# Kernel optimization log

Measured on AMD Instinct MI355X. Metric: run time of the kernel, lower is better.

Reference implementation:

```python
import jax, jax.numpy as jnp
import numpy as np

B, S, D, H = 8, 1024, 768, 12
DH = D // H  # 64


def setup_inputs() -> dict:
    key = jax.random.key(0)
    ks = jax.random.split(key, 7)
    scale = 0.05
    return {
        "sequences": jax.random.normal(ks[0], (B, S, D), dtype=jnp.float32),
        "Wq": jax.random.normal(ks[1], (H, DH, DH), dtype=jnp.float32) * scale,
        "bq": jax.random.normal(ks[2], (H, DH), dtype=jnp.float32) * scale,
        "Wk": jax.random.normal(ks[3], (H, DH, DH), dtype=jnp.float32) * scale,
        "bk": jax.random.normal(ks[4], (H, DH), dtype=jnp.float32) * scale,
        "Wv": jax.random.normal(ks[5], (H, DH, DH), dtype=jnp.float32) * scale,
        "bv": jax.random.normal(ks[6], (H, DH), dtype=jnp.float32) * scale,
    }


def reference(sequences, Wq, bq, Wk, bk, Wv, bv):
    # sequences: [B, S, D]; per-head slice of width DH gets its own Linear.
    b, s, d = sequences.shape
    h, dh = Wq.shape[0], Wq.shape[-1]
    xh = sequences.reshape(b, s, h, dh)  # [B,S,H,DH] head-chunked features
    q = jnp.einsum('bshd,hde->bshe', xh, Wq) + bq  # [B,S,H,DH]
    k = jnp.einsum('bshd,hde->bshe', xh, Wk) + bk
    v = jnp.einsum('bshd,hde->bshe', xh, Wv) + bv
    scores = jnp.einsum('bqhd,bkhd->bhqk', q, k) / jnp.sqrt(jnp.float32(dh))
    weights = jax.nn.softmax(scores, axis=-1)  # [B,H,S,S]
    out = jnp.einsum('bhqk,bkhd->bqhd', weights, v)  # [B,S,H,DH]
    return out.reshape(b, s, d)  # hstack of heads == reshape back to D
```

## Files before the change

### kernel.cpp

```cpp
#include <hip/hip_runtime.h>
#include <hip/hip_bf16.h>
#include <math.h>

constexpr int Bn = 8, Sn = 1024, Dn = 768, Hn = 12, DHn = 64;
constexpr int QKV_ELEMS = Bn * Hn * Sn * DHn;
constexpr float SQC = 0.42466086f;

typedef __attribute__((ext_vector_type(8))) short bf16x8;
typedef __attribute__((ext_vector_type(4))) float f32x4;

__device__ __forceinline__ unsigned short f2bf(float f) {
    union { float f; unsigned u; } c{f};
    return (unsigned short)((c.u + 0x8000) >> 16);
}
__device__ __forceinline__ unsigned int pk2bf(float a, float b) {
    union { float f; unsigned u; } ca{a}, cb{b};
    return __builtin_amdgcn_perm(cb.u + 0x8000u, ca.u + 0x8000u, 0x07060302u);
}

__global__ __launch_bounds__(256) void prep_kernel(
    const float* __restrict__ Wq, const float* __restrict__ Wk,
    const float* __restrict__ Wv, unsigned short* __restrict__ wt_g)
{
    __shared__ float Ws[64][65];
    const int mh = blockIdx.x;
    const int m  = mh / Hn;
    const int h  = mh % Hn;
    const float* W = (m == 0 ? Wq : (m == 1 ? Wk : Wv)) + (size_t)h * 4096;
    const int t  = threadIdx.x;
    const int r  = t >> 2;
    const int c0 = (t & 3) * 16;
    #pragma unroll
    for (int q4 = 0; q4 < 4; q4++) {
        float4 v = ((const float4*)(W + r * 64 + c0))[q4];
        Ws[r][c0 + 4 * q4 + 0] = v.x;
        Ws[r][c0 + 4 * q4 + 1] = v.y;
        Ws[r][c0 + 4 * q4 + 2] = v.z;
        Ws[r][c0 + 4 * q4 + 3] = v.w;
    }
    __syncthreads();
    const int e  = t >> 2;
    const int d0 = (t & 3) * 16;
    const float sc = (m < 2) ? SQC : 1.0f;
    unsigned short tmp[16];
    #pragma unroll
    for (int j = 0; j < 16; j++) tmp[j] = f2bf(Ws[d0 + j][e] * sc);
    uint4* dst = (uint4*)(wt_g + ((size_t)(mh * 64 + e)) * 64 + d0);
    dst[0] = ((uint4*)tmp)[0];
    dst[1] = ((uint4*)tmp)[1];
}

__global__ __launch_bounds__(256) void proj_kernel(
    const float* __restrict__ x, const unsigned short* __restrict__ wt_g,
    const float* __restrict__ bk, const float* __restrict__ bv,
    unsigned short* __restrict__ k_ws, unsigned short* __restrict__ vt_ws)
{
    __shared__ unsigned short Xs[64 * 72];
    __shared__ unsigned short ObK[64 * 72];
    __shared__ unsigned short ObV[64 * 72];

    const int blk  = blockIdx.x;
    const int tile = blk & 15;
    const int bh   = blk >> 4;
    const int h    = bh % Hn;
    const int b    = bh / Hn;
    const int t    = threadIdx.x;
    const int w    = t >> 6;
    const int lane = t & 63;
    const int l    = lane & 15;
    const int quad = lane >> 4;
    const int r    = t >> 2;
    const int c0   = (t & 3) * 16;
    const int s0   = tile * 64;

    {
        const float* xrow = x + ((size_t)(b * Sn + s0 + r) * Dn + h * 64 + c0);
        unsigned int tmp[8];
        #pragma unroll
        for (int q4 = 0; q4 < 4; q4++) {
            float4 v = ((const float4*)xrow)[q4];
            tmp[2 * q4 + 0] = pk2bf(v.x, v.y);
            tmp[2 * q4 + 1] = pk2bf(v.z, v.w);
        }
        *(uint4*)&Xs[r * 72 + c0]     = ((uint4*)tmp)[0];
        *(uint4*)&Xs[r * 72 + c0 + 8] = ((uint4*)tmp)[1];
    }

    bf16x8 wk[2], wv[2];
    {
        const unsigned short* kp = wt_g + ((size_t)((1 * Hn + h) * 64 + w * 16 + l)) * 64 + quad * 8;
        const unsigned short* vp = wt_g + ((size_t)((2 * Hn + h) * 64 + w * 16 + l)) * 64 + quad * 8;
        uint4 a0 = *(const uint4*)kp;      uint4 a1 = *(const uint4*)(kp + 32);
        uint4 b0 = *(const uint4*)vp;      uint4 b1 = *(const uint4*)(vp + 32);
        wk[0] = *(bf16x8*)&a0; wk[1] = *(bf16x8*)&a1;
        wv[0] = *(bf16x8*)&b0; wv[1] = *(bf16x8*)&b1;
    }
    float4 bkv = *(const float4*)(bk + h * 64 + w * 16 + quad * 4);
    float4 bvv = *(const float4*)(bv + h * 64 + w * 16 + quad * 4);

    __syncthreads();

    bf16x8 xb[4][2];
    #pragma unroll
    for (int nt = 0; nt < 4; nt++)
        #pragma unroll
        for (int kc = 0; kc < 2; kc++)
            xb[nt][kc] = *(bf16x8*)&Xs[(nt * 16 + l) * 72 + kc * 32 + quad * 8];

    f32x4 ak[4], av[4];
    #pragma unroll
    for (int nt = 0; nt < 4; nt++) {
        ak[nt] = (f32x4){bkv.x * SQC, bkv.y * SQC, bkv.z * SQC, bkv.w * SQC};
        av[nt] = (f32x4){bvv.x, bvv.y, bvv.z, bvv.w};
    }
    #pragma unroll
    for (int nt = 0; nt < 4; nt++)
        #pragma unroll
        for (int kc = 0; kc < 2; kc++) {
            ak[nt] = __builtin_amdgcn_mfma_f32_16x16x32_bf16(wk[kc], xb[nt][kc], ak[nt], 0, 0, 0);
            av[nt] = __builtin_amdgcn_mfma_f32_16x16x32_bf16(wv[kc], xb[nt][kc], av[nt], 0, 0, 0);
        }

    #pragma unroll
    for (int nt = 0; nt < 4; nt++) {
        *(uint2*)&ObK[(nt * 16 + l) * 72 + w * 16 + quad * 4] =
            make_uint2(pk2bf(ak[nt][0], ak[nt][1]), pk2bf(ak[nt][2], ak[nt][3]));
        #pragma unroll
        for (int rr = 0; rr < 4; rr++)
            ObV[(w * 16 + quad * 4 + rr) * 72 + nt * 16 + l] = f2bf(av[nt][rr]);
    }
    __syncthreads();

    {
        uint4 a = *(uint4*)&ObK[r * 72 + c0];
        uint4 bq4 = *(uint4*)&ObK[r * 72 + c0 + 8];
        unsigned short* dst = k_ws + (size_t)(bh * Sn + s0 + r) * 64 + c0;
        ((uint4*)dst)[0] = a;
        *(uint4*)(dst + 8) = bq4;
    }
    {
        uint4 a = *(uint4*)&ObV[r * 72 + c0];
        uint4 bq4 = *(uint4*)&ObV[r * 72 + c0 + 8];
        unsigned short* dst = vt_ws + (size_t)bh * 64 * Sn + (size_t)r * Sn + s0 + c0;
        ((uint4*)dst)[0] = a;
        *(uint4*)(dst + 8) = bq4;
    }
}

__global__ __launch_bounds__(256) void attn_kernel(
    const float* __restrict__ x, const unsigned short* __restrict__ wt_g,
    const float* __restrict__ bq,
    const unsigned short* __restrict__ k_ws,
    const unsigned short* __restrict__ vt_ws,
    float* __restrict__ out)
{
    __shared__ unsigned short Ks[64 * 72];
    __shared__ unsigned short Vt[64 * 72];
    __shared__ unsigned short Pws[4 * 32 * 72];

    const int blk = blockIdx.x;
    const int xcd = blk & 7;
    const int idx = blk >> 3;
    const int bh  = xcd * 12 + (idx % 12);
    const int qt  = idx / 12;
    const int t    = threadIdx.x;
    const int w    = t >> 6;
    const int lane = t & 63;
    const int l    = lane & 15;
    const int quad = lane >> 4;
    const int sr   = t >> 2;
    const int sc0  = (t & 3) * 16;

    const int b = bh / Hn, h = bh % Hn;
    const size_t base  = (size_t)bh * Sn * 64;
    const size_t vbase = (size_t)bh * 64 * Sn;

    unsigned short* Pw = Pws + w * 32 * 72;

    bf16x8 qf[2][2];
    {
        bf16x8 xq[2][2];
        #pragma unroll
        for (int st = 0; st < 2; st++) {
            const float* xp = x + ((size_t)(b * Sn + qt * 128 + w * 32 + st * 16 + l) * Dn
                                   + h * 64 + quad * 8);
            #pragma unroll
            for (int kc = 0; kc < 2; kc++) {
                float4 v0 = *(const float4*)(xp + kc * 32);
                float4 v1 = *(const float4*)(xp + kc * 32 + 4);
                unsigned int tmp[4] = {pk2bf(v0.x, v0.y), pk2bf(v0.z, v0.w),
                                       pk2bf(v1.x, v1.y), pk2bf(v1.z, v1.w)};
                xq[st][kc] = *(bf16x8*)tmp;
            }
        }
        #pragma unroll
        for (int nt = 0; nt < 4; nt++) {
            const unsigned short* wp = wt_g + ((size_t)((0 * Hn + h) * 64 + nt * 16 + l)) * 64 + quad * 8;
            uint4 a0 = *(const uint4*)wp;
            uint4 a1 = *(const uint4*)(wp + 32);
            bf16x8 wa0 = *(bf16x8*)&a0, wa1 = *(bf16x8*)&a1;
            float4 bqv = *(const float4*)(bq + h * 64 + nt * 16 + quad * 4);
            #pragma unroll
            for (int st = 0; st < 2; st++) {
                f32x4 acc = (f32x4){bqv.x * SQC, bqv.y * SQC, bqv.z * SQC, bqv.w * SQC};
                acc = __builtin_amdgcn_mfma_f32_16x16x32_bf16(wa0, xq[st][0], acc, 0, 0, 0);
                acc = __builtin_amdgcn_mfma_f32_16x16x32_bf16(wa1, xq[st][1], acc, 0, 0, 0);
                *(uint2*)&Pw[(st * 16 + l) * 72 + nt * 16 + quad * 4] =
                    make_uint2(pk2bf(acc[0], acc[1]), pk2bf(acc[2], acc[3]));
            }
        }
        __asm__ volatile("s_waitcnt lgkmcnt(0)" ::: "memory");
        #pragma unroll
        for (int st = 0; st < 2; st++) {
            qf[st][0] = *(bf16x8*)&Pw[(st * 16 + l) * 72 + quad * 8];
            qf[st][1] = *(bf16x8*)&Pw[(st * 16 + l) * 72 + 32 + quad * 8];
        }
    }

    f32x4 Oa[2][4];
    #pragma unroll
    for (int st = 0; st < 2; st++)
        #pragma unroll
        for (int nt = 0; nt < 4; nt++) Oa[st][nt] = (f32x4){0.f, 0.f, 0.f, 0.f};
    float ps[2] = {0.f, 0.f};

    for (int kt = 0; kt < 16; kt++) {
        __syncthreads();
        {
            const unsigned short* kp = k_ws + base + (size_t)(kt * 64 + sr) * 64 + sc0;
            uint4 ka = *(const uint4*)kp;
            uint4 kb = *(const uint4*)(kp + 8);
            const unsigned short* vp = vt_ws + vbase + (size_t)sr * Sn + kt * 64 + sc0;
            uint4 va = *(const uint4*)vp;
            uint4 vb = *(const uint4*)(vp + 8);
            *(uint4*)&Ks[sr * 72 + sc0]     = ka;
            *(uint4*)&Ks[sr * 72 + sc0 + 8] = kb;
            *(uint4*)&Vt[sr * 72 + sc0]     = va;
            *(uint4*)&Vt[sr * 72 + sc0 + 8] = vb;
        }
        __syncthreads();

        #pragma unroll
        for (int nt = 0; nt < 4; nt++) {
            bf16x8 kf0 = *(bf16x8*)&Ks[(nt * 16 + l) * 72 + quad * 8];
            bf16x8 kf1 = *(bf16x8*)&Ks[(nt * 16 + l) * 72 + 32 + quad * 8];
            #pragma unroll
            for (int st = 0; st < 2; st++) {
                f32x4 s = (f32x4){0.f, 0.f, 0.f, 0.f};
                s = __builtin_amdgcn_mfma_f32_16x16x32_bf16(kf0, qf[st][0], s, 0, 0, 0);
                s = __builtin_amdgcn_mfma_f32_16x16x32_bf16(kf1, qf[st][1], s, 0, 0, 0);
                float p0 = exp2f(s[0]), p1 = exp2f(s[1]);
                float p2 = exp2f(s[2]), p3 = exp2f(s[3]);
                ps[st] += (p0 + p1) + (p2 + p3);
                *(uint2*)&Pw[(st * 16 + l) * 72 + nt * 16 + quad * 4] =
                    make_uint2(pk2bf(p0, p1), pk2bf(p2, p3));
            }
        }
        __asm__ volatile("s_waitcnt lgkmcnt(0)" ::: "memory");

        bf16x8 pf[2][2];
        #pragma unroll
        for (int st = 0; st < 2; st++) {
            pf[st][0] = *(bf16x8*)&Pw[(st * 16 + l) * 72 + quad * 8];
            pf[st][1] = *(bf16x8*)&Pw[(st * 16 + l) * 72 + 32 + quad * 8];
        }

        #pragma unroll
        for (int nt = 0; nt < 4; nt++) {
            bf16x8 vf0 = *(bf16x8*)&Vt[(nt * 16 + l) * 72 + quad * 8];
            bf16x8 vf1 = *(bf16x8*)&Vt[(nt * 16 + l) * 72 + 32 + quad * 8];
            #pragma unroll
            for (int st = 0; st < 2; st++) {
                Oa[st][nt] = __builtin_amdgcn_mfma_f32_16x16x32_bf16(pf[st][0], vf0, Oa[st][nt], 0, 0, 0);
                Oa[st][nt] = __builtin_amdgcn_mfma_f32_16x16x32_bf16(pf[st][1], vf1, Oa[st][nt], 0, 0, 0);
            }
        }
    }

    #pragma unroll
    for (int st = 0; st < 2; st++) {
        ps[st] += __shfl_xor(ps[st], 16, 64);
        ps[st] += __shfl_xor(ps[st], 32, 64);
    }

    #pragma unroll
    for (int st = 0; st < 2; st++) {
        float inv[4];
        #pragma unroll
        for (int r = 0; r < 4; r++) inv[r] = 1.0f / __shfl(ps[st], quad * 4 + r, 64);
        #pragma unroll
        for (int nt = 0; nt < 4; nt++)
            #pragma unroll
            for (int r = 0; r < 4; r++) {
                int srow = qt * 128 + w * 32 + st * 16 + quad * 4 + r;
                out[(size_t)(b * Sn + srow) * Dn + h * 64 + nt * 16 + l] = Oa[st][nt][r] * inv[r];
            }
    }
}

extern "C" void kernel_launch(void* const* d_in, const int* in_sizes, int n_in,
                              void* d_out, int out_size, void* d_ws, size_t ws_size,
                              hipStream_t stream) {
    const float* x  = (const float*)d_in[0];
    const float* Wq = (const float*)d_in[1];
    const float* bq = (const float*)d_in[2];
    const float* Wk = (const float*)d_in[3];
    const float* bk = (const float*)d_in[4];
    const float* Wv = (const float*)d_in[5];
    const float* bv = (const float*)d_in[6];
    float* out = (float*)d_out;

    unsigned short* k_ws  = (unsigned short*)d_ws;
    unsigned short* vt_ws = k_ws + QKV_ELEMS;
    unsigned short* wt_g  = vt_ws + QKV_ELEMS;

    hipLaunchKernelGGL(prep_kernel, dim3(3 * Hn), dim3(256), 0, stream,
                       Wq, Wk, Wv, wt_g);
    hipLaunchKernelGGL(proj_kernel, dim3(Bn * Hn * 16), dim3(256), 0, stream,
                       x, wt_g, bk, bv, k_ws, vt_ws);
    hipLaunchKernelGGL(attn_kernel, dim3(Bn * Hn * 8), dim3(256), 0, stream,
                       x, wt_g, bq, k_ws, vt_ws, out);
}
```

Before: 143.6 us.

## Fuse K/V projection into attention kernel, recomputing per key tile

```diff
diff --git a/kernel.cpp b/kernel.cpp
--- a/kernel.cpp
+++ b/kernel.cpp
@@ -3,7 +3,6 @@
 #include <math.h>
 
 constexpr int Bn = 8, Sn = 1024, Dn = 768, Hn = 12, DHn = 64;
-constexpr int QKV_ELEMS = Bn * Hn * Sn * DHn;
 constexpr float SQC = 0.42466086f;
 
 typedef __attribute__((ext_vector_type(8))) short bf16x8;
@@ -50,110 +49,13 @@
     dst[1] = ((uint4*)tmp)[1];
 }
 
-__global__ __launch_bounds__(256) void proj_kernel(
+__global__ __launch_bounds__(256) void attn_kernel(
     const float* __restrict__ x, const unsigned short* __restrict__ wt_g,
-    const float* __restrict__ bk, const float* __restrict__ bv,
-    unsigned short* __restrict__ k_ws, unsigned short* __restrict__ vt_ws)
+    const float* __restrict__ bq, const float* __restrict__ bk,
+    const float* __restrict__ bv,
+    float* __restrict__ out)
 {
     __shared__ unsigned short Xs[64 * 72];
-    __shared__ unsigned short ObK[64 * 72];
-    __shared__ unsigned short ObV[64 * 72];
-
-    const int blk  = blockIdx.x;
-    const int tile = blk & 15;
-    const int bh   = blk >> 4;
-    const int h    = bh % Hn;
-    const int b    = bh / Hn;
-    const int t    = threadIdx.x;
-    const int w    = t >> 6;
-    const int lane = t & 63;
-    const int l    = lane & 15;
-    const int quad = lane >> 4;
-    const int r    = t >> 2;
-    const int c0   = (t & 3) * 16;
-    const int s0   = tile * 64;
-
-    {
-        const float* xrow = x + ((size_t)(b * Sn + s0 + r) * Dn + h * 64 + c0);
-        unsigned int tmp[8];
-        #pragma unroll
-        for (int q4 = 0; q4 < 4; q4++) {
-            float4 v = ((const float4*)xrow)[q4];
-            tmp[2 * q4 + 0] = pk2bf(v.x, v.y);
-            tmp[2 * q4 + 1] = pk2bf(v.z, v.w);
-        }
-        *(uint4*)&Xs[r * 72 + c0]     = ((uint4*)tmp)[0];
-        *(uint4*)&Xs[r * 72 + c0 + 8] = ((uint4*)tmp)[1];
-    }
-
-    bf16x8 wk[2], wv[2];
-    {
-        const unsigned short* kp = wt_g + ((size_t)((1 * Hn + h) * 64 + w * 16 + l)) * 64 + quad * 8;
-        const unsigned short* vp = wt_g + ((size_t)((2 * Hn + h) * 64 + w * 16 + l)) * 64 + quad * 8;
-        uint4 a0 = *(const uint4*)kp;      uint4 a1 = *(const uint4*)(kp + 32);
-        uint4 b0 = *(const uint4*)vp;      uint4 b1 = *(const uint4*)(vp + 32);
-        wk[0] = *(bf16x8*)&a0; wk[1] = *(bf16x8*)&a1;
-        wv[0] = *(bf16x8*)&b0; wv[1] = *(bf16x8*)&b1;
-    }
-    float4 bkv = *(const float4*)(bk + h * 64 + w * 16 + quad * 4);
-    float4 bvv = *(const float4*)(bv + h * 64 + w * 16 + quad * 4);
-
-    __syncthreads();
-
-    bf16x8 xb[4][2];
-    #pragma unroll
-    for (int nt = 0; nt < 4; nt++)
-        #pragma unroll
-        for (int kc = 0; kc < 2; kc++)
-            xb[nt][kc] = *(bf16x8*)&Xs[(nt * 16 + l) * 72 + kc * 32 + quad * 8];
-
-    f32x4 ak[4], av[4];
-    #pragma unroll
-    for (int nt = 0; nt < 4; nt++) {
-        ak[nt] = (f32x4){bkv.x * SQC, bkv.y * SQC, bkv.z * SQC, bkv.w * SQC};
-        av[nt] = (f32x4){bvv.x, bvv.y, bvv.z, bvv.w};
-    }
-    #pragma unroll
-    for (int nt = 0; nt < 4; nt++)
-        #pragma unroll
-        for (int kc = 0; kc < 2; kc++) {
-            ak[nt] = __builtin_amdgcn_mfma_f32_16x16x32_bf16(wk[kc], xb[nt][kc], ak[nt], 0, 0, 0);
-            av[nt] = __builtin_amdgcn_mfma_f32_16x16x32_bf16(wv[kc], xb[nt][kc], av[nt], 0, 0, 0);
-        }
-
-    #pragma unroll
-    for (int nt = 0; nt < 4; nt++) {
-        *(uint2*)&ObK[(nt * 16 + l) * 72 + w * 16 + quad * 4] =
-            make_uint2(pk2bf(ak[nt][0], ak[nt][1]), pk2bf(ak[nt][2], ak[nt][3]));
-        #pragma unroll
-        for (int rr = 0; rr < 4; rr++)
-            ObV[(w * 16 + quad * 4 + rr) * 72 + nt * 16 + l] = f2bf(av[nt][rr]);
-    }
-    __syncthreads();
-
-    {
-        uint4 a = *(uint4*)&ObK[r * 72 + c0];
-        uint4 bq4 = *(uint4*)&ObK[r * 72 + c0 + 8];
-        unsigned short* dst = k_ws + (size_t)(bh * Sn + s0 + r) * 64 + c0;
-        ((uint4*)dst)[0] = a;
-        *(uint4*)(dst + 8) = bq4;
-    }
-    {
-        uint4 a = *(uint4*)&ObV[r * 72 + c0];
-        uint4 bq4 = *(uint4*)&ObV[r * 72 + c0 + 8];
-        unsigned short* dst = vt_ws + (size_t)bh * 64 * Sn + (size_t)r * Sn + s0 + c0;
-        ((uint4*)dst)[0] = a;
-        *(uint4*)(dst + 8) = bq4;
-    }
-}
-
-__global__ __launch_bounds__(256) void attn_kernel(
-    const float* __restrict__ x, const unsigned short* __restrict__ wt_g,
-    const float* __restrict__ bq,
-    const unsigned short* __restrict__ k_ws,
-    const unsigned short* __restrict__ vt_ws,
-    float* __restrict__ out)
-{
     __shared__ unsigned short Ks[64 * 72];
     __shared__ unsigned short Vt[64 * 72];
     __shared__ unsigned short Pws[4 * 32 * 72];
@@ -172,10 +74,20 @@
     const int sc0  = (t & 3) * 16;
 
     const int b = bh / Hn, h = bh % Hn;
-    const size_t base  = (size_t)bh * Sn * 64;
-    const size_t vbase = (size_t)bh * 64 * Sn;
-
     unsigned short* Pw = Pws + w * 32 * 72;
+
+    bf16x8 wk[2], wv[2];
+    {
+        const unsigned short* kp = wt_g + ((size_t)((1 * Hn + h) * 64 + w * 16 + l)) * 64 + quad * 8;
+        const unsigned short* vp = wt_g + ((size_t)((2 * Hn + h) * 64 + w * 16 + l)) * 64 + quad * 8;
+        uint4 a0 = *(const uint4*)kp;  uint4 a1 = *(const uint4*)(kp + 32);
+        uint4 b0 = *(const uint4*)vp;  uint4 b1 = *(const uint4*)(vp + 32);
+        wk[0] = *(bf16x8*)&a0; wk[1] = *(bf16x8*)&a1;
+        wv[0] = *(bf16x8*)&b0; wv[1] = *(bf16x8*)&b1;
+    }
+    float4 bkv = *(const float4*)(bk + h * 64 + w * 16 + quad * 4);
+    bkv.x *= SQC; bkv.y *= SQC; bkv.z *= SQC; bkv.w *= SQC;
+    const float bvl = bv[h * 64 + w * 16 + l];
 
     bf16x8 qf[2][2];
     {
@@ -227,16 +139,40 @@
     for (int kt = 0; kt < 16; kt++) {
         __syncthreads();
         {
-            const unsigned short* kp = k_ws + base + (size_t)(kt * 64 + sr) * 64 + sc0;
-            uint4 ka = *(const uint4*)kp;
-            uint4 kb = *(const uint4*)(kp + 8);
-            const unsigned short* vp = vt_ws + vbase + (size_t)sr * Sn + kt * 64 + sc0;
-            uint4 va = *(const uint4*)vp;
-            uint4 vb = *(const uint4*)(vp + 8);
-            *(uint4*)&Ks[sr * 72 + sc0]     = ka;
-            *(uint4*)&Ks[sr * 72 + sc0 + 8] = kb;
-            *(uint4*)&Vt[sr * 72 + sc0]     = va;
-            *(uint4*)&Vt[sr * 72 + sc0 + 8] = vb;
+            const float* xrow = x + ((size_t)(b * Sn + kt * 64 + sr) * Dn + h * 64 + sc0);
+            unsigned int tmp[8];
+            #pragma unroll
+            for (int q4 = 0; q4 < 4; q4++) {
+                float4 v = ((const float4*)xrow)[q4];
+                tmp[2 * q4 + 0] = pk2bf(v.x, v.y);
+                tmp[2 * q4 + 1] = pk2bf(v.z, v.w);
+            }
+            *(uint4*)&Xs[sr * 72 + sc0]     = ((uint4*)tmp)[0];
+            *(uint4*)&Xs[sr * 72 + sc0 + 8] = ((uint4*)tmp)[1];
+        }
+        __syncthreads();
+
+        {
+            bf16x8 xf[4][2];
+            #pragma unroll
+            for (int nt = 0; nt < 4; nt++)
+                #pragma unroll
+                for (int kc = 0; kc < 2; kc++)
+                    xf[nt][kc] = *(bf16x8*)&Xs[(nt * 16 + l) * 72 + kc * 32 + quad * 8];
+
+            #pragma unroll
+            for (int nt = 0; nt < 4; nt++) {
+                f32x4 ak = (f32x4){bkv.x, bkv.y, bkv.z, bkv.w};
+                ak = __builtin_amdgcn_mfma_f32_16x16x32_bf16(wk[0], xf[nt][0], ak, 0, 0, 0);
+                ak = __builtin_amdgcn_mfma_f32_16x16x32_bf16(wk[1], xf[nt][1], ak, 0, 0, 0);
+                *(uint2*)&Ks[(nt * 16 + l) * 72 + w * 16 + quad * 4] =
+                    make_uint2(pk2bf(ak[0], ak[1]), pk2bf(ak[2], ak[3]));
+                f32x4 av = (f32x4){bvl, bvl, bvl, bvl};
+                av = __builtin_amdgcn_mfma_f32_16x16x32_bf16(xf[nt][0], wv[0], av, 0, 0, 0);
+                av = __builtin_amdgcn_mfma_f32_16x16x32_bf16(xf[nt][1], wv[1], av, 0, 0, 0);
+                *(uint2*)&Vt[(w * 16 + l) * 72 + nt * 16 + quad * 4] =
+                    make_uint2(pk2bf(av[0], av[1]), pk2bf(av[2], av[3]));
+            }
         }
         __syncthreads();
 
@@ -310,14 +246,10 @@
     const float* bv = (const float*)d_in[6];
     float* out = (float*)d_out;
 
-    unsigned short* k_ws  = (unsigned short*)d_ws;
-    unsigned short* vt_ws = k_ws + QKV_ELEMS;
-    unsigned short* wt_g  = vt_ws + QKV_ELEMS;
+    unsigned short* wt_g = (unsigned short*)d_ws;
 
     hipLaunchKernelGGL(prep_kernel, dim3(3 * Hn), dim3(256), 0, stream,
                        Wq, Wk, Wv, wt_g);
-    hipLaunchKernelGGL(proj_kernel, dim3(Bn * Hn * 16), dim3(256), 0, stream,
-                       x, wt_g, bk, bv, k_ws, vt_ws);
     hipLaunchKernelGGL(attn_kernel, dim3(Bn * Hn * 8), dim3(256), 0, stream,
-                       x, wt_g, bq, k_ws, vt_ws, out);
-}
+                       x, wt_g, bq, bk, bv, out);
+}
```

New measurement: 169.7 us. 18.1% more time.
